# Optimization experiments

Hardware: AMD Instinct MI355X
Metric: run time of the kernel (lower is better)

## Reference

```python
import jax, jax.numpy as jnp
import numpy as np

L, B, E, H, HID = 2048, 4, 512, 8, 2048
HD = E // H


def setup_inputs() -> dict:
    key = jax.random.key(0)
    ks = jax.random.split(key, 6)
    s = 0.02
    x = jax.random.normal(ks[0], (L, B, E), jnp.float32)
    in_proj_w = jax.random.normal(ks[1], (3 * E, E), jnp.float32) * s
    in_proj_b = jnp.zeros((3 * E,), jnp.float32)
    out_w = jax.random.normal(ks[2], (E, E), jnp.float32) * s
    out_b = jnp.zeros((E,), jnp.float32)
    w1 = jax.random.normal(ks[3], (HID, E), jnp.float32) * s  # torch Linear: (out, in)
    b1 = jnp.zeros((HID,), jnp.float32)
    w2 = jax.random.normal(ks[4], (E, HID), jnp.float32) * s
    b2 = jnp.zeros((E,), jnp.float32)
    ln_g = jnp.ones((E,), jnp.float32)
    ln_b = jnp.zeros((E,), jnp.float32)
    return {"x": x, "in_proj_w": in_proj_w, "in_proj_b": in_proj_b,
            "out_w": out_w, "out_b": out_b, "w1": w1, "b1": b1,
            "w2": w2, "b2": b2, "ln_g": ln_g, "ln_b": ln_b}


def _pos_encoding(S, Emb, dtype):
    # even i: sin((t+1) * 10000^(-i/E)); odd i: cos((t+1) * 10000^(-(i+1)/E))
    t = jnp.arange(S, dtype=dtype)[:, None]
    i = jnp.arange(Emb, dtype=dtype)[None, :]
    even = jnp.sin((t + 1.0) * jnp.power(10000.0, -i / Emb))
    odd = jnp.cos((t + 1.0) * jnp.power(10000.0, -(i + 1.0) / Emb))
    return jnp.where(jnp.arange(Emb)[None, :] % 2 == 0, even, odd)  # (S, Emb)


def _layernorm(x, g, b, eps=1e-5):
    mu = jnp.mean(x, axis=-1, keepdims=True)
    var = jnp.mean(jnp.square(x - mu), axis=-1, keepdims=True)
    return (x - mu) * jax.lax.rsqrt(var + eps) * g + b


def _mha(x, in_proj_w, in_proj_b, out_w, out_b):
    # x: (L, B, E); self-attention, torch MultiheadAttention semantics
    qkv = jnp.einsum('lbe,fe->lbf', x, in_proj_w) + in_proj_b
    q, k, v = jnp.split(qkv, 3, axis=-1)
    q = q.reshape(L, B, H, HD)
    k = k.reshape(L, B, H, HD)
    v = v.reshape(L, B, H, HD)
    scores = jnp.einsum('lbhd,mbhd->bhlm', q, k) / np.sqrt(HD).astype(np.float32)
    attn = jax.nn.softmax(scores, axis=-1)
    o = jnp.einsum('bhlm,mbhd->lbhd', attn, v).reshape(L, B, E)
    return jnp.einsum('lbe,fe->lbf', o, out_w) + out_b


def reference(x, in_proj_w, in_proj_b, out_w, out_b, w1, b1, w2, b2, ln_g, ln_b):
    # positional encoding: varies along dim1, broadcasts along dim0 (as in source)
    pe = _pos_encoding(x.shape[1], x.shape[2], x.dtype)  # (B, E)
    x = x + pe[None, :, :]
    # Post-Norm path
    x = _layernorm(_mha(x, in_proj_w, in_proj_b, out_w, out_b) + x, ln_g, ln_b)
    h = jax.nn.gelu(jnp.einsum('lbe,he->lbh', x, w1) + b1, approximate=False)
    ff = jnp.einsum('lbh,eh->lbe', h, w2) + b2
    x = _layernorm(ff + x, ln_g, ln_b)
    return x
```

## Files before the change

kernel.cpp:

```cpp
#include <hip/hip_runtime.h>

typedef unsigned short u16;
typedef unsigned int   u32;
typedef u16  u16x2 __attribute__((ext_vector_type(2)));
typedef u16  u16x4 __attribute__((ext_vector_type(4)));
typedef u16  u16x8 __attribute__((ext_vector_type(8)));
typedef short s8v  __attribute__((ext_vector_type(8)));
typedef float f4v  __attribute__((ext_vector_type(4)));
typedef u32  u32x2 __attribute__((ext_vector_type(2)));
typedef u32  u32x4 __attribute__((ext_vector_type(4)));

#define L_SEQ 2048
#define B_SZ  4
#define E_DIM 512
#define H_CNT 8
#define HD    64
#define HID   2048
#define M_ROWS (L_SEQ * B_SZ)
#define QSCALE 0.18033688011112042f

__device__ __forceinline__ u16 f2b(float f) {
    unsigned u = __builtin_bit_cast(unsigned, f);
    u += 0x7fffu + ((u >> 16) & 1u);
    return (u16)(u >> 16);
}
__device__ __forceinline__ float b2f(u16 u) {
    u32 x = ((u32)u) << 16; return __builtin_bit_cast(float, x);
}
#if defined(__has_builtin)
#if __has_builtin(__builtin_amdgcn_cvt_pk_bf16_f32)
#define HAVE_PK_BF16 1
#endif
#if __has_builtin(__builtin_amdgcn_rcpf)
#define HAVE_RCPF 1
#endif
#endif
__device__ __forceinline__ u32 pk_trunc(float a, float b) {
#ifdef HAVE_PK_BF16
    typedef __bf16 bf2 __attribute__((ext_vector_type(2)));
    bf2 r = __builtin_amdgcn_cvt_pk_bf16_f32(a, b);
    return __builtin_bit_cast(u32, r);
#else
    u32 ua = __builtin_bit_cast(u32, a), ub = __builtin_bit_cast(u32, b);
    return (ua >> 16) | (ub & 0xffff0000u);
#endif
}
__device__ __forceinline__ float frcp(float x) {
#ifdef HAVE_RCPF
    return __builtin_amdgcn_rcpf(x);
#else
    return 1.0f / x;
#endif
}
__device__ __forceinline__ void gload_lds16(const u16* g, u16* l) {
    __builtin_amdgcn_global_load_lds((__attribute__((address_space(1))) void*)(u16*)g,
                                     (__attribute__((address_space(3))) void*)l, 16, 0, 0);
}
__device__ __forceinline__ float gelu_f(float v) {
    float y2 = v * (1.5957691216f + 0.0713548576f * v * v);
    return v / (1.0f + __expf(-y2));
}

__global__ __launch_bounds__(256) void pe_tab_k(float* __restrict__ pet) {
    int i = blockIdx.x * 256 + threadIdx.x;
    int e = i & (E_DIM - 1);
    float t = (float)(i >> 9) + 1.0f;
    int ee = (e & 1) ? (e + 1) : e;
    float w = exp2f((-(float)ee / 512.0f) * 13.287712379549449f);
    pet[i] = (e & 1) ? cosf(t * w) : sinf(t * w);
}

__global__ __launch_bounds__(256) void prep_k(const float* __restrict__ x,
                                              const float* __restrict__ pet,
                                              u16* __restrict__ xpb,
                                              const float* __restrict__ s1, u16* __restrict__ d1, int n1,
                                              const float* __restrict__ s2, u16* __restrict__ d2, int n2,
                                              const float* __restrict__ s3, u16* __restrict__ d3, int n3,
                                              const float* __restrict__ s4, u16* __restrict__ d4) {
    int bid = blockIdx.x;
    if (bid < 4096) {
        int idx = (bid * 256 + threadIdx.x) * 4;
        f4v v = *(const f4v*)(x + idx);
        f4v p = *(const f4v*)(pet + (idx & 2047));
        u16x4 o;
#pragma unroll
        for (int i = 0; i < 4; ++i) o[i] = f2b(v[i] + p[i]);
        *(u16x4*)(xpb + idx) = o;
    } else {
        int o = ((bid - 4096) * 256 + threadIdx.x) * 4;
        const float* s; u16* d;
        if (o < n1) { s = s1; d = d1; }
        else { o -= n1;
            if (o < n2) { s = s2; d = d2; }
            else { o -= n2;
                if (o < n3) { s = s3; d = d3; }
                else { o -= n3; s = s4; d = d4; } } }
        f4v v = *(const f4v*)(s + o);
        u16x4 q;
#pragma unroll
        for (int i = 0; i < 4; ++i) q[i] = f2b(v[i]);
        *(u16x4*)(d + o) = q;
    }
}

template <int NP, bool WRITEF, bool WRITEB>
__global__ __launch_bounds__(256)
void ln_c(const u16* __restrict__ p0, const u16* __restrict__ p1,
          const u16* __restrict__ p2, const u16* __restrict__ p3,
          const float* __restrict__ bias, const u16* __restrict__ resid,
          const float* __restrict__ gw, const float* __restrict__ bw,
          float* __restrict__ outF, u16* __restrict__ outB) {
    int wave = threadIdx.x >> 6, lane = threadIdx.x & 63;
    size_t row = (size_t)blockIdx.x * 4 + wave;
    size_t off = row * E_DIM + lane * 8;
    u16x8 rv = *(const u16x8*)(resid + off);
    f4v a, b;
#pragma unroll
    for (int i = 0; i < 4; ++i) { a[i] = b2f(rv[i]); b[i] = b2f(rv[i + 4]); }
    a += *(const f4v*)(bias + lane * 8);
    b += *(const f4v*)(bias + lane * 8 + 4);
    const u16* ps[4] = {p0, p1, p2, p3};
#pragma unroll
    for (int z = 0; z < NP; ++z) {
        u16x8 t = *(const u16x8*)(ps[z] + off);
#pragma unroll
        for (int i = 0; i < 4; ++i) { a[i] += b2f(t[i]); b[i] += b2f(t[i + 4]); }
    }
    float s = (a[0] + a[1]) + (a[2] + a[3]) + (b[0] + b[1]) + (b[2] + b[3]);
#pragma unroll
    for (int o = 1; o < 64; o <<= 1) s += __shfl_xor(s, o, 64);
    float mu = s * (1.0f / E_DIM);
    float q = 0.f;
#pragma unroll
    for (int i = 0; i < 4; ++i) { float d = a[i] - mu; q += d * d; }
#pragma unroll
    for (int i = 0; i < 4; ++i) { float d = b[i] - mu; q += d * d; }
#pragma unroll
    for (int o = 1; o < 64; o <<= 1) q += __shfl_xor(q, o, 64);
    float rstd = rsqrtf(q * (1.0f / E_DIM) + 1e-5f);
    f4v g0 = *(const f4v*)(gw + lane * 8), g1 = *(const f4v*)(gw + lane * 8 + 4);
    f4v w0 = *(const f4v*)(bw + lane * 8), w1 = *(const f4v*)(bw + lane * 8 + 4);
    f4v y0, y1;
#pragma unroll
    for (int i = 0; i < 4; ++i) { y0[i] = (a[i] - mu) * rstd * g0[i] + w0[i];
                                  y1[i] = (b[i] - mu) * rstd * g1[i] + w1[i]; }
    if (WRITEF) {
        *(f4v*)(outF + off)     = y0;
        *(f4v*)(outF + off + 4) = y1;
    }
    if (WRITEB) {
        u16x8 o;
#pragma unroll
        for (int i = 0; i < 4; ++i) { o[i] = f2b(y0[i]); o[i + 4] = f2b(y1[i]); }
        *(u16x8*)(outB + off) = o;
    }
}

__global__ __launch_bounds__(256, 4)
void gemm_ks(const u16* __restrict__ A, const u16* __restrict__ Bw,
             int N, int K, int Kper,
             u16* __restrict__ q0, u16* __restrict__ q1) {
    __shared__ __align__(16) u16 As[2][128 * 32];
    __shared__ __align__(16) u16 Bs[2][128 * 32];
    const int tid = threadIdx.x;
    const int wave = tid >> 6, lane = tid & 63;
    const int col = lane & 15, quad = lane >> 4;
    const int n = blockIdx.x;
    const int xcd = n & 7, loc = n >> 3;
    const int bn = (loc & 3) * 128;
    const int bm = (xcd * 8 + ((loc >> 2) & 7)) * 128;
    const int kz = loc >> 5;
    u16* pz = kz ? q1 : q0;
    const int wm = (wave >> 1) * 64, wn = (wave & 1) * 64;
    f4v acc[4][4] = {};
    const int srow = wave * 16 + (lane >> 2);
    const int soff = (lane & 3) * 8;
    const u16* Ag = A + (size_t)(bm + srow) * K + kz * Kper + soff;
    const u16* Bg = Bw + (size_t)(bn + srow) * K + kz * Kper + soff;
    const int wo = wave * 512;
    gload_lds16(Ag,                  &As[0][wo]);
    gload_lds16(Ag + (size_t)64 * K, &As[0][wo + 2048]);
    gload_lds16(Bg,                  &Bs[0][wo]);
    gload_lds16(Bg + (size_t)64 * K, &Bs[0][wo + 2048]);
    const int nit = Kper >> 5;
    for (int t = 0; t < nit; ++t) {
        const int cur = t & 1, nxt = cur ^ 1;
        __syncthreads();
        if (t + 1 < nit) {
            const int kc = (t + 1) * 32;
            gload_lds16(Ag + kc,                  &As[nxt][wo]);
            gload_lds16(Ag + (size_t)64 * K + kc, &As[nxt][wo + 2048]);
            gload_lds16(Bg + kc,                  &Bs[nxt][wo]);
            gload_lds16(Bg + (size_t)64 * K + kc, &Bs[nxt][wo + 2048]);
        }
        s8v af[4], bf[4];
#pragma unroll
        for (int i = 0; i < 4; ++i) af[i] = *(const s8v*)(&As[cur][(wm + i * 16 + col) * 32 + quad * 8]);
#pragma unroll
        for (int j = 0; j < 4; ++j) bf[j] = *(const s8v*)(&Bs[cur][(wn + j * 16 + col) * 32 + quad * 8]);
#pragma unroll
        for (int i = 0; i < 4; ++i)
#pragma unroll
            for (int j = 0; j < 4; ++j)
                acc[i][j] = __builtin_amdgcn_mfma_f32_16x16x32_bf16(af[i], bf[j], acc[i][j], 0, 0, 0);
    }
#pragma unroll
    for (int j = 0; j < 4; ++j) {
        int gn = bn + wn + j * 16 + col;
#pragma unroll
        for (int i = 0; i < 4; ++i) {
            int m0 = bm + wm + i * 16 + quad * 4;
#pragma unroll
            for (int r = 0; r < 4; ++r)
                pz[(size_t)(m0 + r) * N + gn] = f2b(acc[i][j][r]);
        }
    }
}

#define G28_STAGE(Ad, Bd, kf)                                                          \
    {                                                                                  \
        _Pragma("unroll")                                                              \
        for (int s = 0; s < 2; ++s) {                                                  \
            const int qa = s * 512 + tid;                                              \
            const int rhoA = qa >> 2;                                                  \
            gload_lds16(A + (size_t)(bm + rhoA) * Ka + koff + (kf) + gsw, (Ad) + qa * 8); \
        }                                                                              \
        {                                                                              \
            const int rhoB = tid >> 2;                                                 \
            gload_lds16(Bw + (size_t)(bn + rhoB) * Kb + koff + (kf) + gsw, (Bd) + tid * 8); \
        }                                                                              \
    }

#define G28_COMPUTE(Ab_, Bb_)                                                          \
    {                                                                                  \
        s8v bfr[4], afr[4];                                                            \
        _Pragma("unroll")                                                              \
        for (int j = 0; j < 4; ++j) {                                                  \
            const int rB = wc * 64 + j * 16 + col;                                     \
            bfr[j] = *(const s8v*)((Bb_) + rB * 32 + ((quad ^ ((rB >> 1) & 3)) * 8));  \
        }                                                                              \
        _Pragma("unroll")                                                              \
        for (int i = 0; i < 4; ++i) {                                                  \
            const int rA = wr * 64 + i * 16 + col;                                     \
            afr[i] = *(const s8v*)((Ab_) + rA * 32 + ((quad ^ ((rA >> 1) & 3)) * 8));  \
        }                                                                              \
        __builtin_amdgcn_s_setprio(1);                                                 \
        _Pragma("unroll")                                                              \
        for (int i = 0; i < 4; ++i)                                                    \
            _Pragma("unroll")                                                          \
            for (int j = 0; j < 4; ++j)                                                \
                acc[i][j] = __builtin_amdgcn_mfma_f32_16x16x32_bf16(afr[i], bfr[j], acc[i][j], 0, 0, 0); \
        __builtin_amdgcn_s_setprio(0);                                                 \
    }

template <int MODE, int NTL, int KZL, int KTILES>
__global__ __launch_bounds__(512, 2)
void g28(const u16* __restrict__ A, const u16* __restrict__ Bw,
         const float* __restrict__ bias, int Ka, int Kb, int N,
         u16* __restrict__ o0, u16* __restrict__ o1, u16* __restrict__ o2) {
    extern __shared__ __align__(16) u16 LDS[];
    const int tid = threadIdx.x;
    const int wave = tid >> 6, lane = tid & 63;
    const int col = lane & 15, quad = lane >> 4;
    const int wr = wave >> 1, wc = wave & 1;
    const int n = blockIdx.x;
    const int xcd = n & 7, loc = n >> 3;
    const int mt = xcd * 4 + (loc & 3);
    const int rest = loc >> 2;
    const int nt = (NTL == 1) ? 0 : (rest % NTL);
    const int kz = (KZL == 1) ? 0 : (rest / NTL);
    const int bm = mt * 256, bn = nt * 128;
    const int koff = kz * (KTILES * 32);
    const int gsw = ((lane & 3) ^ ((lane >> 3) & 3)) * 8;
    f4v acc[4][4] = {};
    u16* A0 = LDS;          u16* B0 = LDS + 8192;
    u16* A1 = LDS + 12288;  u16* B1 = LDS + 20480;
    u16* A2 = LDS + 24576;  u16* B2 = LDS + 32768;
    G28_STAGE(A0, B0, 0);
    G28_STAGE(A1, B1, 32);
    asm volatile("s_waitcnt vmcnt(3)" ::: "memory");
    __builtin_amdgcn_s_barrier();
    __builtin_amdgcn_sched_barrier(0);
    for (int t = 0; t < KTILES - 2; ++t) {
        G28_STAGE(A2, B2, (t + 2) * 32);
        G28_COMPUTE(A0, B0);
        asm volatile("s_waitcnt vmcnt(3)" ::: "memory");
        __builtin_amdgcn_s_barrier();
        __builtin_amdgcn_sched_barrier(0);
        u16* ta = A0; A0 = A1; A1 = A2; A2 = ta;
        u16* tb = B0; B0 = B1; B1 = B2; B2 = tb;
    }
    G28_COMPUTE(A0, B0);
    asm volatile("s_waitcnt vmcnt(0)" ::: "memory");
    __builtin_amdgcn_s_barrier();
    __builtin_amdgcn_sched_barrier(0);
    G28_COMPUTE(A1, B1);
    if (MODE == 0 && nt >= 8) {
        __syncthreads();
        u16* xb = LDS;
#pragma unroll
        for (int j = 0; j < 4; ++j) {
            const int ln = wc * 64 + j * 16 + col;
            const float bv = bias[nt * 128 + ln];
#pragma unroll
            for (int i = 0; i < 4; ++i) {
                const int lm = wr * 64 + i * 16 + quad * 4;
#pragma unroll
                for (int r = 0; r < 4; ++r)
                    xb[ln * 264 + lm + r] = f2b(acc[i][j][r] + bv);
            }
        }
        __syncthreads();
        const int l0 = bm >> 2;
        for (int rr = 0; rr < 64; ++rr) {
            const int rid = wave * 64 + rr;
            const int ln = rid >> 2, b = rid & 3;
            const int h = (nt - 8) * 2 + (ln >> 6), d = ln & 63;
            u16 v = xb[ln * 264 + lane * 4 + b];
            o2[((size_t)(b * H_CNT + h) * HD + d) * L_SEQ + l0 + lane] = v;
        }
        return;
    }
#pragma unroll
    for (int j = 0; j < 4; ++j) {
        const int gn = bn + wc * 64 + j * 16 + col;
        if (MODE == 0) {
            const float bv = bias[gn];
            const int which = gn >> 9, hh = (gn >> 6) & 7, d = gn & 63;
            u16* dst = (which == 0) ? o0 : o1;
            const float qs = (which == 0) ? QSCALE : 1.0f;
#pragma unroll
            for (int i = 0; i < 4; ++i) {
                const int m0 = bm + wr * 64 + i * 16 + quad * 4;
#pragma unroll
                for (int r = 0; r < 4; ++r) {
                    const int m = m0 + r;
                    const int l = m >> 2, bb = m & 3;
                    dst[((size_t)(bb * H_CNT + hh) * L_SEQ + l) * HD + d] = f2b((acc[i][j][r] + bv) * qs);
                }
            }
        } else if (MODE == 2) {
            const float bv = bias[gn];
#pragma unroll
            for (int i = 0; i < 4; ++i) {
                const int m0 = bm + wr * 64 + i * 16 + quad * 4;
#pragma unroll
                for (int r = 0; r < 4; ++r)
                    o0[(size_t)(m0 + r) * N + gn] = f2b(gelu_f(acc[i][j][r] + bv));
            }
        } else {
            u16* pz = (kz == 0) ? o0 : o1;
#pragma unroll
            for (int i = 0; i < 4; ++i) {
                const int m0 = bm + wr * 64 + i * 16 + quad * 4;
#pragma unroll
                for (int r = 0; r < 4; ++r)
                    pz[(size_t)(m0 + r) * N + gn] = f2b(acc[i][j][r]);
            }
        }
    }
}

__global__ __launch_bounds__(512, 4)
void attn_k(const u16* __restrict__ qg, const u16* __restrict__ kg,
            const u16* __restrict__ vtg, u16* __restrict__ og) {
    __shared__ __align__(16) u16 KV[2][2][2][2][64 * 32];
    __shared__ float LSB[2][256];
    const int tid = threadIdx.x;
    const int wave = tid >> 6, lane = tid & 63;
    const int grp = wave >> 2, w4 = wave & 3;
    const int col = lane & 15, quad = lane >> 4;
    const int flat = blockIdx.x;
    const int xcd = flat & 7, loc = flat >> 3;
    const int bh = xcd * 4 + (loc >> 4);
    const int qc = loc & 15;
    const size_t base = (size_t)bh * (L_SEQ * HD);
    s8v qf[2][2];
#pragma unroll
    for (int t = 0; t < 2; ++t) {
        const int qrow = qc * 128 + w4 * 32 + t * 16 + col;
#pragma unroll
        for (int hh = 0; hh < 2; ++hh)
            qf[t][hh] = *(const s8v*)(qg + base + (size_t)qrow * HD + hh * 32 + quad * 8);
    }
    f4v oa[2][4] = {};
    float ls0 = 0.f, ls1 = 0.f;
    const int h = w4 & 1, r0 = (w4 >> 1) * 16;
    const int srow = lane >> 2, c = lane & 3;
    const int cp = c ^ ((srow >> 1) & 3);
    const int sig = ((srow >> 2) << 3) + ((r0 >> 4) << 2) + (srow & 3);
    const u16* Kg = kg + base + (size_t)(sig + grp * 1024) * HD + h * 32 + cp * 8;
    const u16* Vg = vtg + base + (size_t)(r0 + srow) * L_SEQ + grp * 1024 + h * 32 + cp * 8;
    {
        gload_lds16(Kg,                      &KV[grp][0][0][h][r0 * 32]);
        gload_lds16(Kg + (size_t)32 * HD,    &KV[grp][0][0][h][(r0 + 32) * 32]);
        gload_lds16(Vg,                      &KV[grp][1][0][h][r0 * 32]);
        gload_lds16(Vg + (size_t)32 * L_SEQ, &KV[grp][1][0][h][(r0 + 32) * 32]);
    }
    const int perm = (col >> 1) & 3;
    for (int it = 0; it < 16; ++it) {
        const int cur = it & 1, nxt = cur ^ 1;
        __syncthreads();
        if (it + 1 < 16) {
            const int kv0 = (it + 1) * 64;
            gload_lds16(Kg + (size_t)kv0 * HD,         &KV[grp][0][nxt][h][r0 * 32]);
            gload_lds16(Kg + (size_t)(kv0 + 32) * HD,  &KV[grp][0][nxt][h][(r0 + 32) * 32]);
            gload_lds16(Vg + kv0,                      &KV[grp][1][nxt][h][r0 * 32]);
            gload_lds16(Vg + kv0 + (size_t)32 * L_SEQ, &KV[grp][1][nxt][h][(r0 + 32) * 32]);
        }
        f4v st[2][4];
#pragma unroll
        for (int j = 0; j < 4; ++j) {
            s8v k0 = *(const s8v*)(&KV[grp][0][cur][0][(j * 16 + col) * 32 + ((quad ^ perm) * 8)]);
            s8v k1 = *(const s8v*)(&KV[grp][0][cur][1][(j * 16 + col) * 32 + ((quad ^ perm) * 8)]);
#pragma unroll
            for (int t = 0; t < 2; ++t) {
                f4v z = {};
                z = __builtin_amdgcn_mfma_f32_16x16x32_bf16(k0, qf[t][0], z, 0, 0, 0);
                z = __builtin_amdgcn_mfma_f32_16x16x32_bf16(k1, qf[t][1], z, 0, 0, 0);
                st[t][j] = z;
            }
        }
        u32 pk[2][4][2];
#pragma unroll
        for (int t = 0; t < 2; ++t)
#pragma unroll
            for (int j = 0; j < 4; ++j) {
                f4v p;
#pragma unroll
                for (int r = 0; r < 4; ++r) p[r] = __builtin_amdgcn_exp2f(st[t][j][r]);
                float psum = (p[0] + p[1]) + (p[2] + p[3]);
                if (t == 0) ls0 += psum; else ls1 += psum;
                pk[t][j][0] = pk_trunc(p[0], p[1]);
                pk[t][j][1] = pk_trunc(p[2], p[3]);
            }
#pragma unroll
        for (int c2 = 0; c2 < 2; ++c2) {
            s8v pf[2];
#pragma unroll
            for (int t = 0; t < 2; ++t) {
                u32x4 q4 = {pk[t][2 * c2][0], pk[t][2 * c2][1],
                            pk[t][2 * c2 + 1][0], pk[t][2 * c2 + 1][1]};
                pf[t] = __builtin_bit_cast(s8v, q4);
            }
#pragma unroll
            for (int dj = 0; dj < 4; ++dj) {
                s8v vf = *(const s8v*)(&KV[grp][1][cur][c2][(dj * 16 + col) * 32 + ((quad ^ perm) * 8)]);
#pragma unroll
                for (int t = 0; t < 2; ++t)
                    oa[t][dj] = __builtin_amdgcn_mfma_f32_16x16x32_bf16(pf[t], vf, oa[t][dj], 0, 0, 0);
            }
        }
    }
    ls0 += __shfl_xor(ls0, 16, 64); ls0 += __shfl_xor(ls0, 32, 64);
    ls1 += __shfl_xor(ls1, 16, 64); ls1 += __shfl_xor(ls1, 32, 64);
    float* cmb = (float*)&KV[1][0][0][0][0];
    const int slot = w4 * 64 + lane;
    if (grp == 1) {
#pragma unroll
        for (int t = 0; t < 2; ++t)
#pragma unroll
            for (int dj = 0; dj < 4; ++dj)
                *(f4v*)(cmb + ((size_t)(t * 4 + dj) * 256 + slot) * 4) = oa[t][dj];
        LSB[0][slot] = ls0;
        LSB[1][slot] = ls1;
    }
    __syncthreads();
    if (grp == 0) {
#pragma unroll
        for (int t = 0; t < 2; ++t)
#pragma unroll
            for (int dj = 0; dj < 4; ++dj)
                oa[t][dj] += *(const f4v*)(cmb + ((size_t)(t * 4 + dj) * 256 + slot) * 4);
        ls0 += LSB[0][slot];
        ls1 += LSB[1][slot];
        const int b = bh >> 3, hd = bh & 7;
#pragma unroll
        for (int t = 0; t < 2; ++t)
#pragma unroll
            for (int r = 0; r < 4; ++r) {
                float lv = __shfl(t == 0 ? ls0 : ls1, quad * 4 + r, 64);
                float inv = frcp(lv);
                int lrow = qc * 128 + w4 * 32 + t * 16 + quad * 4 + r;
                size_t mrow = (size_t)(lrow * 4 + b) * E_DIM + hd * HD;
#pragma unroll
                for (int dj = 0; dj < 4; ++dj)
                    og[mrow + dj * 16 + col] = f2b(oa[t][dj][r] * inv);
            }
    }
}

extern "C" void kernel_launch(void* const* d_in, const int* in_sizes, int n_in,
                              void* d_out, int out_size, void* d_ws, size_t ws_size,
                              hipStream_t stream) {
    const float* x     = (const float*)d_in[0];
    const float* w_qkv = (const float*)d_in[1];
    const float* b_qkv = (const float*)d_in[2];
    const float* w_out = (const float*)d_in[3];
    const float* b_out = (const float*)d_in[4];
    const float* w1    = (const float*)d_in[5];
    const float* b1    = (const float*)d_in[6];
    const float* w2    = (const float*)d_in[7];
    const float* b2    = (const float*)d_in[8];
    const float* ln_g  = (const float*)d_in[9];
    const float* ln_b  = (const float*)d_in[10];

    char* ws = (char*)d_ws;
    u16*   WQKV = (u16*)(ws + 0);
    u16*   WOUT = (u16*)(ws + 1572864);
    u16*   W1B  = (u16*)(ws + 2097152);
    u16*   W2B  = (u16*)(ws + 4194304);
    u16*   XPB  = (u16*)(ws + 6291456);
    u16*   QB   = (u16*)(ws + 14680064);
    u16*   KB   = (u16*)(ws + 23068672);
    u16*   VB   = (u16*)(ws + 31457280);
    u16*   VT   = (u16*)(ws + 39845888);
    float* PET  = (float*)(ws + 82837504);
    u16*   OB   = VB;
    u16*   OP0  = (u16*)(ws + 48234496);
    u16*   OP1  = (u16*)(ws + 56623104);
    u16*   X3B  = QB;
    u16*   HB   = (u16*)(ws + 48234496);
    u16*   FP0  = XPB;
    u16*   FP1  = KB;

    static bool attr_done = false;
    if (!attr_done) {
        hipFuncSetAttribute((const void*)g28<0, 12, 1, 16>,
                            hipFuncAttributeMaxDynamicSharedMemorySize, 73728);
        hipFuncSetAttribute((const void*)g28<2, 16, 1, 16>,
                            hipFuncAttributeMaxDynamicSharedMemorySize, 73728);
        hipFuncSetAttribute((const void*)g28<3, 4, 2, 32>,
                            hipFuncAttributeMaxDynamicSharedMemorySize, 73728);
        attr_done = true;
    }

    pe_tab_k<<<8, 256, 0, stream>>>(PET);
    prep_k<<<7168, 256, 0, stream>>>(x, PET, XPB,
                                     w_qkv, WQKV, 3 * E_DIM * E_DIM,
                                     w_out, WOUT, E_DIM * E_DIM,
                                     w1, W1B, HID * E_DIM,
                                     w2, W2B);
    g28<0, 12, 1, 16><<<384, 512, 73728, stream>>>(XPB, WQKV, b_qkv, E_DIM, E_DIM, 0,
                                                   QB, KB, VT);
    attn_k<<<512, 512, 0, stream>>>(QB, KB, VT, OB);
    gemm_ks<<<512, 256, 0, stream>>>(OB, WOUT, E_DIM, E_DIM, 256, OP0, OP1);
    ln_c<2, false, true><<<2048, 256, 0, stream>>>(OP0, OP1, nullptr, nullptr,
                                                   b_out, XPB, ln_g, ln_b, nullptr, X3B);
    g28<2, 16, 1, 16><<<512, 512, 73728, stream>>>(X3B, W1B, b1, E_DIM, E_DIM, HID,
                                                   HB, nullptr, nullptr);
    g28<3, 4, 2, 32><<<256, 512, 73728, stream>>>(HB, W2B, nullptr, HID, HID, E_DIM,
                                                  FP0, FP1, nullptr);
    ln_c<2, true, false><<<2048, 256, 0, stream>>>(FP0, FP1, nullptr, nullptr,
                                                   b2, X3B, ln_g, ln_b, (float*)d_out, nullptr);
}
```

Baseline: 223.7 us.

## Widen attention KV tiles to 128 and reuse g28 for out-projection

```diff
diff --git a/kernel.cpp b/kernel.cpp
--- a/kernel.cpp
+++ b/kernel.cpp
@@ -153,67 +153,6 @@
 #pragma unroll
         for (int i = 0; i < 4; ++i) { o[i] = f2b(y0[i]); o[i + 4] = f2b(y1[i]); }
         *(u16x8*)(outB + off) = o;
-    }
-}
-
-__global__ __launch_bounds__(256, 4)
-void gemm_ks(const u16* __restrict__ A, const u16* __restrict__ Bw,
-             int N, int K, int Kper,
-             u16* __restrict__ q0, u16* __restrict__ q1) {
-    __shared__ __align__(16) u16 As[2][128 * 32];
-    __shared__ __align__(16) u16 Bs[2][128 * 32];
-    const int tid = threadIdx.x;
-    const int wave = tid >> 6, lane = tid & 63;
-    const int col = lane & 15, quad = lane >> 4;
-    const int n = blockIdx.x;
-    const int xcd = n & 7, loc = n >> 3;
-    const int bn = (loc & 3) * 128;
-    const int bm = (xcd * 8 + ((loc >> 2) & 7)) * 128;
-    const int kz = loc >> 5;
-    u16* pz = kz ? q1 : q0;
-    const int wm = (wave >> 1) * 64, wn = (wave & 1) * 64;
-    f4v acc[4][4] = {};
-    const int srow = wave * 16 + (lane >> 2);
-    const int soff = (lane & 3) * 8;
-    const u16* Ag = A + (size_t)(bm + srow) * K + kz * Kper + soff;
-    const u16* Bg = Bw + (size_t)(bn + srow) * K + kz * Kper + soff;
-    const int wo = wave * 512;
-    gload_lds16(Ag,                  &As[0][wo]);
-    gload_lds16(Ag + (size_t)64 * K, &As[0][wo + 2048]);
-    gload_lds16(Bg,                  &Bs[0][wo]);
-    gload_lds16(Bg + (size_t)64 * K, &Bs[0][wo + 2048]);
-    const int nit = Kper >> 5;
-    for (int t = 0; t < nit; ++t) {
-        const int cur = t & 1, nxt = cur ^ 1;
-        __syncthreads();
-        if (t + 1 < nit) {
-            const int kc = (t + 1) * 32;
-            gload_lds16(Ag + kc,                  &As[nxt][wo]);
-            gload_lds16(Ag + (size_t)64 * K + kc, &As[nxt][wo + 2048]);
-            gload_lds16(Bg + kc,                  &Bs[nxt][wo]);
-            gload_lds16(Bg + (size_t)64 * K + kc, &Bs[nxt][wo + 2048]);
-        }
-        s8v af[4], bf[4];
-#pragma unroll
-        for (int i = 0; i < 4; ++i) af[i] = *(const s8v*)(&As[cur][(wm + i * 16 + col) * 32 + quad * 8]);
-#pragma unroll
-        for (int j = 0; j < 4; ++j) bf[j] = *(const s8v*)(&Bs[cur][(wn + j * 16 + col) * 32 + quad * 8]);
-#pragma unroll
-        for (int i = 0; i < 4; ++i)
-#pragma unroll
-            for (int j = 0; j < 4; ++j)
-                acc[i][j] = __builtin_amdgcn_mfma_f32_16x16x32_bf16(af[i], bf[j], acc[i][j], 0, 0, 0);
-    }
-#pragma unroll
-    for (int j = 0; j < 4; ++j) {
-        int gn = bn + wn + j * 16 + col;
-#pragma unroll
-        for (int i = 0; i < 4; ++i) {
-            int m0 = bm + wm + i * 16 + quad * 4;
-#pragma unroll
-            for (int r = 0; r < 4; ++r)
-                pz[(size_t)(m0 + r) * N + gn] = f2b(acc[i][j][r]);
-        }
     }
 }
 
@@ -361,11 +300,10 @@
     }
 }
 
-__global__ __launch_bounds__(512, 4)
+__global__ __launch_bounds__(512, 1)
 void attn_k(const u16* __restrict__ qg, const u16* __restrict__ kg,
             const u16* __restrict__ vtg, u16* __restrict__ og) {
-    __shared__ __align__(16) u16 KV[2][2][2][2][64 * 32];
-    __shared__ float LSB[2][256];
+    extern __shared__ __align__(16) u16 ALDS[];
     const int tid = threadIdx.x;
     const int wave = tid >> 6, lane = tid & 63;
     const int grp = wave >> 2, w4 = wave & 3;
@@ -388,31 +326,35 @@
     const int h = w4 & 1, r0 = (w4 >> 1) * 16;
     const int srow = lane >> 2, c = lane & 3;
     const int cp = c ^ ((srow >> 1) & 3);
-    const int sig = ((srow >> 2) << 3) + ((r0 >> 4) << 2) + (srow & 3);
-    const u16* Kg = kg + base + (size_t)(sig + grp * 1024) * HD + h * 32 + cp * 8;
-    const u16* Vg = vtg + base + (size_t)(r0 + srow) * L_SEQ + grp * 1024 + h * 32 + cp * 8;
-    {
-        gload_lds16(Kg,                      &KV[grp][0][0][h][r0 * 32]);
-        gload_lds16(Kg + (size_t)32 * HD,    &KV[grp][0][0][h][(r0 + 32) * 32]);
-        gload_lds16(Vg,                      &KV[grp][1][0][h][r0 * 32]);
-        gload_lds16(Vg + (size_t)32 * L_SEQ, &KV[grp][1][0][h][(r0 + 32) * 32]);
-    }
+    const int sig0 = ((srow >> 2) << 3) + ((r0 >> 4) << 2) + (srow & 3);
+    const u16* Kg = kg + base + (size_t)(sig0 + grp * 1024) * HD + h * 32 + cp * 8;
+    const u16* Vg = vtg + base + (size_t)srow * L_SEQ + grp * 1024 + w4 * 32 + cp * 8;
+    u16* KsG = ALDS + grp * 16384 + h * 4096;
+    u16* VsG = ALDS + 32768 + grp * 16384 + w4 * 2048;
+#define ATTN_STAGE(BUF, KV0)                                                            \
+    {                                                                                   \
+        _Pragma("unroll")                                                               \
+        for (int a = 0; a < 4; ++a) {                                                   \
+            gload_lds16(Kg + (size_t)((KV0) + 64 * (a >> 1) + 32 * (a & 1)) * HD,       \
+                        KsG + (BUF) * 8192 + (r0 + 32 * a) * 32);                       \
+            gload_lds16(Vg + (size_t)(a * 16) * L_SEQ + (KV0),                          \
+                        VsG + (BUF) * 8192 + (a * 16) * 32);                            \
+        }                                                                               \
+    }
+    ATTN_STAGE(0, 0);
     const int perm = (col >> 1) & 3;
-    for (int it = 0; it < 16; ++it) {
+    for (int it = 0; it < 8; ++it) {
         const int cur = it & 1, nxt = cur ^ 1;
         __syncthreads();
-        if (it + 1 < 16) {
-            const int kv0 = (it + 1) * 64;
-            gload_lds16(Kg + (size_t)kv0 * HD,         &KV[grp][0][nxt][h][r0 * 32]);
-            gload_lds16(Kg + (size_t)(kv0 + 32) * HD,  &KV[grp][0][nxt][h][(r0 + 32) * 32]);
-            gload_lds16(Vg + kv0,                      &KV[grp][1][nxt][h][r0 * 32]);
-            gload_lds16(Vg + kv0 + (size_t)32 * L_SEQ, &KV[grp][1][nxt][h][(r0 + 32) * 32]);
-        }
-        f4v st[2][4];
-#pragma unroll
-        for (int j = 0; j < 4; ++j) {
-            s8v k0 = *(const s8v*)(&KV[grp][0][cur][0][(j * 16 + col) * 32 + ((quad ^ perm) * 8)]);
-            s8v k1 = *(const s8v*)(&KV[grp][0][cur][1][(j * 16 + col) * 32 + ((quad ^ perm) * 8)]);
+        if (it + 1 < 8) { ATTN_STAGE(nxt, (it + 1) * 128); }
+        const u16* K0 = ALDS + grp * 16384 + cur * 8192;
+        const u16* K1 = K0 + 4096;
+        f4v st[2][8];
+#pragma unroll
+        for (int j = 0; j < 8; ++j) {
+            const int row = (j >> 2) * 64 + (j & 3) * 16 + col;
+            s8v k0 = *(const s8v*)(K0 + row * 32 + ((quad ^ perm) * 8));
+            s8v k1 = *(const s8v*)(K1 + row * 32 + ((quad ^ perm) * 8));
 #pragma unroll
             for (int t = 0; t < 2; ++t) {
                 f4v z = {};
@@ -421,11 +363,11 @@
                 st[t][j] = z;
             }
         }
-        u32 pk[2][4][2];
+        u32 pk[2][8][2];
 #pragma unroll
         for (int t = 0; t < 2; ++t)
 #pragma unroll
-            for (int j = 0; j < 4; ++j) {
+            for (int j = 0; j < 8; ++j) {
                 f4v p;
 #pragma unroll
                 for (int r = 0; r < 4; ++r) p[r] = __builtin_amdgcn_exp2f(st[t][j][r]);
@@ -435,7 +377,7 @@
                 pk[t][j][1] = pk_trunc(p[2], p[3]);
             }
 #pragma unroll
-        for (int c2 = 0; c2 < 2; ++c2) {
+        for (int c2 = 0; c2 < 4; ++c2) {
             s8v pf[2];
 #pragma unroll
             for (int t = 0; t < 2; ++t) {
@@ -443,18 +385,21 @@
                             pk[t][2 * c2 + 1][0], pk[t][2 * c2 + 1][1]};
                 pf[t] = __builtin_bit_cast(s8v, q4);
             }
+            const u16* Vb = ALDS + 32768 + grp * 16384 + cur * 8192 + c2 * 2048;
 #pragma unroll
             for (int dj = 0; dj < 4; ++dj) {
-                s8v vf = *(const s8v*)(&KV[grp][1][cur][c2][(dj * 16 + col) * 32 + ((quad ^ perm) * 8)]);
+                s8v vf = *(const s8v*)(Vb + (dj * 16 + col) * 32 + ((quad ^ perm) * 8));
 #pragma unroll
                 for (int t = 0; t < 2; ++t)
                     oa[t][dj] = __builtin_amdgcn_mfma_f32_16x16x32_bf16(pf[t], vf, oa[t][dj], 0, 0, 0);
             }
         }
     }
+#undef ATTN_STAGE
     ls0 += __shfl_xor(ls0, 16, 64); ls0 += __shfl_xor(ls0, 32, 64);
     ls1 += __shfl_xor(ls1, 16, 64); ls1 += __shfl_xor(ls1, 32, 64);
-    float* cmb = (float*)&KV[1][0][0][0][0];
+    float* cmb = (float*)(ALDS + 16384);
+    float* LSB = (float*)(ALDS + 65536);
     const int slot = w4 * 64 + lane;
     if (grp == 1) {
 #pragma unroll
@@ -462,8 +407,8 @@
 #pragma unroll
             for (int dj = 0; dj < 4; ++dj)
                 *(f4v*)(cmb + ((size_t)(t * 4 + dj) * 256 + slot) * 4) = oa[t][dj];
-        LSB[0][slot] = ls0;
-        LSB[1][slot] = ls1;
+        LSB[slot] = ls0;
+        LSB[256 + slot] = ls1;
     }
     __syncthreads();
     if (grp == 0) {
@@ -472,8 +417,8 @@
 #pragma unroll
             for (int dj = 0; dj < 4; ++dj)
                 oa[t][dj] += *(const f4v*)(cmb + ((size_t)(t * 4 + dj) * 256 + slot) * 4);
-        ls0 += LSB[0][slot];
-        ls1 += LSB[1][slot];
+        ls0 += LSB[slot];
+        ls1 += LSB[256 + slot];
         const int b = bh >> 3, hd = bh & 7;
 #pragma unroll
         for (int t = 0; t < 2; ++t)
@@ -532,6 +477,10 @@
                             hipFuncAttributeMaxDynamicSharedMemorySize, 73728);
         hipFuncSetAttribute((const void*)g28<3, 4, 2, 32>,
                             hipFuncAttributeMaxDynamicSharedMemorySize, 73728);
+        hipFuncSetAttribute((const void*)g28<3, 4, 2, 8>,
+                            hipFuncAttributeMaxDynamicSharedMemorySize, 73728);
+        hipFuncSetAttribute((const void*)attn_k,
+                            hipFuncAttributeMaxDynamicSharedMemorySize, 133120);
         attr_done = true;
     }
 
@@ -543,8 +492,9 @@
                                      w2, W2B);
     g28<0, 12, 1, 16><<<384, 512, 73728, stream>>>(XPB, WQKV, b_qkv, E_DIM, E_DIM, 0,
                                                    QB, KB, VT);
-    attn_k<<<512, 512, 0, stream>>>(QB, KB, VT, OB);
-    gemm_ks<<<512, 256, 0, stream>>>(OB, WOUT, E_DIM, E_DIM, 256, OP0, OP1);
+    attn_k<<<512, 512, 133120, stream>>>(QB, KB, VT, OB);
+    g28<3, 4, 2, 8><<<256, 512, 73728, stream>>>(OB, WOUT, nullptr, E_DIM, E_DIM, E_DIM,
+                                                 OP0, OP1, nullptr);
     ln_c<2, false, true><<<2048, 256, 0, stream>>>(OP0, OP1, nullptr, nullptr,
                                                    b_out, XPB, ln_g, ln_b, nullptr, X3B);
     g28<2, 16, 1, 16><<<512, 512, 73728, stream>>>(X3B, W1B, b1, E_DIM, E_DIM, HID,
```

New measurement: 243.4 us. 1.09x slower.
